# Kernel tuning notes

Measured on AMD Instinct MI355X. Metric: run time of the kernel, lower is better.

Reference implementation:

```python
import jax, jax.numpy as jnp
import numpy as np

N_LAYER = 4
N_HEAD = 12
D_MODEL = 768
SEQ_LEN = 2048
VOCAB = 50257
BATCH = 2


def _sinusoid_pe(seq_len, d_model):
    pos = np.arange(seq_len, dtype=np.float32)[:, None]
    div = np.exp(np.arange(0, d_model, 2, dtype=np.float32) * (-np.log(10000.0) / d_model))
    pe = np.zeros((seq_len, d_model), dtype=np.float32)
    pe[:, 0::2] = np.sin(pos * div)
    pe[:, 1::2] = np.cos(pos * div)
    return jnp.asarray(pe[None])  # [1, C, D]


def setup_inputs() -> dict:
    key = jax.random.key(0)
    ks = jax.random.split(key, 12)
    s = 0.02
    return {
        "features": jax.random.randint(ks[0], (BATCH, SEQ_LEN), 0, VOCAB),
        "targets": jax.random.randint(ks[1], (BATCH, SEQ_LEN), 0, VOCAB),
        "tok_embed": jax.random.normal(ks[2], (VOCAB, D_MODEL), jnp.float32) * s,
        "pos_emb": _sinusoid_pe(SEQ_LEN, D_MODEL),
        "ln1_w": jnp.ones((N_LAYER, D_MODEL), jnp.float32),
        "ln1_b": jnp.zeros((N_LAYER, D_MODEL), jnp.float32),
        "attn_w": jax.random.normal(ks[3], (N_LAYER, D_MODEL, 3 * D_MODEL), jnp.float32) * s,
        "attn_b": jnp.zeros((N_LAYER, 3 * D_MODEL), jnp.float32),
        "proj_w": jax.random.normal(ks[4], (N_LAYER, D_MODEL, D_MODEL), jnp.float32) * s,
        "proj_b": jnp.zeros((N_LAYER, D_MODEL), jnp.float32),
        "ln2_w": jnp.ones((N_LAYER, D_MODEL), jnp.float32),
        "ln2_b": jnp.zeros((N_LAYER, D_MODEL), jnp.float32),
        "ffn_w1": jax.random.normal(ks[5], (N_LAYER, D_MODEL, 4 * D_MODEL), jnp.float32) * s,
        "ffn_b1": jnp.zeros((N_LAYER, 4 * D_MODEL), jnp.float32),
        "ffn_w2": jax.random.normal(ks[6], (N_LAYER, 4 * D_MODEL, D_MODEL), jnp.float32) * s,
        "ffn_b2": jnp.zeros((N_LAYER, D_MODEL), jnp.float32),
        "lnf_w": jnp.ones((D_MODEL,), jnp.float32),
        "lnf_b": jnp.zeros((D_MODEL,), jnp.float32),
        "final_w": jax.random.normal(ks[7], (D_MODEL, VOCAB), jnp.float32) * s,
    }


def _layernorm(x, w, b, eps=1e-5):
    mu = jnp.mean(x, axis=-1, keepdims=True)
    var = jnp.var(x, axis=-1, keepdims=True)
    return (x - mu) * jax.lax.rsqrt(var + eps) * w + b


def _attention(x, wqkv, bqkv, wo, bo):
    B, C, E = x.shape
    dh = E // N_HEAD
    qkv = x @ wqkv + bqkv  # [B, C, 3E]
    q, k, v = jnp.split(qkv, 3, axis=-1)
    q = q.reshape(B, C, N_HEAD, dh)
    k = k.reshape(B, C, N_HEAD, dh)
    v = v.reshape(B, C, N_HEAD, dh)
    att = jnp.einsum("bqhd,bkhd->bhqk", q, k) / jnp.sqrt(jnp.float32(dh))
    causal = jnp.tril(jnp.ones((C, C), bool))
    att = jnp.where(causal, att, -jnp.inf)
    att = jax.nn.softmax(att, axis=-1)
    y = jnp.einsum("bhqk,bkhd->bqhd", att, v).reshape(B, C, E)
    return y @ wo + bo


def reference(features, targets, tok_embed, pos_emb, ln1_w, ln1_b, attn_w, attn_b,
              proj_w, proj_b, ln2_w, ln2_b, ffn_w1, ffn_b1, ffn_w2, ffn_b2,
              lnf_w, lnf_b, final_w):
    C = features.shape[1]
    x = tok_embed[features] + pos_emb[:, :C]
    for l in range(N_LAYER):
        h = _layernorm(x, ln1_w[l], ln1_b[l])
        x = x + _attention(h, attn_w[l], attn_b[l], proj_w[l], proj_b[l])
        h = _layernorm(x, ln2_w[l], ln2_b[l])
        h = jax.nn.gelu(h @ ffn_w1[l] + ffn_b1[l], approximate=False) @ ffn_w2[l] + ffn_b2[l]
        x = x + h
    x = _layernorm(x, lnf_w, lnf_b)
    logits = x @ final_w  # [B, C, V]
    logp = jax.nn.log_softmax(logits, axis=-1)
    tgt = targets.reshape(-1)
    valid = tgt != -1
    tgt_safe = jnp.where(valid, tgt, 0)
    nll = -jnp.take_along_axis(logp.reshape(-1, logits.shape[-1]), tgt_safe[:, None], axis=1)[:, 0]
    loss = jnp.sum(jnp.where(valid, nll, 0.0)) / jnp.maximum(jnp.sum(valid), 1)
    return logits, loss
```

## Files before the change

### kernel.cpp

```cpp
#include <hip/hip_runtime.h>
#include <math.h>

#define N_LAYER 4
#define N_HEAD  12
#define D_MODEL 768
#define SEQ     2048
#define VOCAB   50257
#define BATCH   2
#define MROWS   (BATCH*SEQ)

typedef __bf16 bf16;
typedef __bf16 bf16x8 __attribute__((ext_vector_type(8)));
typedef float  f32x4  __attribute__((ext_vector_type(4)));
typedef short  short8v __attribute__((ext_vector_type(8)));

__device__ __forceinline__ void gload16(const bf16* g, const bf16* l) {
    __builtin_amdgcn_global_load_lds(
        (const __attribute__((address_space(1))) void*)g,
        (__attribute__((address_space(3))) void*)l,
        16, 0, 0);
}

__global__ __launch_bounds__(256) void embed_kernel(
    const int* __restrict__ feat, const float* __restrict__ tok,
    const float* __restrict__ pos, float* __restrict__ x)
{
    int row = blockIdx.x;
    int cpos = row & (SEQ - 1);
    int tid = feat[row];
    const float* te = tok + (size_t)tid * D_MODEL;
    const float* pe = pos + (size_t)cpos * D_MODEL;
    float* xr = x + (size_t)row * D_MODEL;
    for (int c = threadIdx.x; c < D_MODEL; c += 256)
        xr[c] = te[c] + pe[c];
}

__global__ __launch_bounds__(256) void ln_kernel(
    const float* __restrict__ x, const float* __restrict__ w,
    const float* __restrict__ b, bf16* __restrict__ out)
{
    int row = blockIdx.x;
    const float* xr = x + (size_t)row * D_MODEL;
    float lv[3];
    float s = 0.f, ss = 0.f;
#pragma unroll
    for (int i = 0; i < 3; i++) {
        float v = xr[threadIdx.x + i * 256];
        lv[i] = v; s += v; ss += v * v;
    }
#pragma unroll
    for (int o = 32; o; o >>= 1) { s += __shfl_down(s, o, 64); ss += __shfl_down(ss, o, 64); }
    __shared__ float red[8];
    int wid = threadIdx.x >> 6;
    if ((threadIdx.x & 63) == 0) { red[wid] = s; red[wid + 4] = ss; }
    __syncthreads();
    s  = red[0] + red[1] + red[2] + red[3];
    ss = red[4] + red[5] + red[6] + red[7];
    float mu  = s * (1.f / D_MODEL);
    float var = ss * (1.f / D_MODEL) - mu * mu;
    float rs  = rsqrtf(var + 1e-5f);
#pragma unroll
    for (int i = 0; i < 3; i++) {
        int c = threadIdx.x + i * 256;
        out[(size_t)row * D_MODEL + c] = (bf16)((lv[i] - mu) * rs * w[c] + b[c]);
    }
}

__global__ __launch_bounds__(256) void transpose_conv_kernel(
    const float* __restrict__ W, bf16* __restrict__ Wt, int K, int N)
{
    int l = blockIdx.z;
    const float* Wl = W + (size_t)l * K * N;
    bf16* Wtl = Wt + (size_t)l * K * N;
    __shared__ float tile[32][33];
    int k0 = blockIdx.y * 32, n0 = blockIdx.x * 32;
    for (int idx = threadIdx.x; idx < 1024; idx += 256) {
        int i = idx >> 5, j = idx & 31;
        int n = n0 + j;
        tile[i][j] = (n < N) ? Wl[(size_t)(k0 + i) * N + n] : 0.f;
    }
    __syncthreads();
    for (int idx = threadIdx.x; idx < 1024; idx += 256) {
        int j = idx >> 5, i = idx & 31;
        int n = n0 + j;
        if (n < N) Wtl[(size_t)n * K + k0 + i] = (bf16)tile[i][j];
    }
}

__global__ __launch_bounds__(256) void vtrans_kernel(
    const bf16* __restrict__ qkv, bf16* __restrict__ vT)
{
    int j0 = blockIdx.x * 64, h = blockIdx.y, b = blockIdx.z;
    __shared__ bf16 t[64][72];
    const bf16* src = qkv + ((size_t)b * SEQ + j0) * (3 * D_MODEL) + 2 * D_MODEL + h * 64;
    int tid = threadIdx.x;
#pragma unroll
    for (int i = 0; i < 2; i++) {
        int c = tid + i * 256;
        int j = c >> 3, d8 = (c & 7) * 8;
        *(short8v*)&t[j][d8] = *(const short8v*)&src[(size_t)j * (3 * D_MODEL) + d8];
    }
    __syncthreads();
    bf16* dst = vT + ((size_t)(b * N_HEAD + h) * 64) * SEQ;
#pragma unroll
    for (int i = 0; i < 2; i++) {
        int c = tid + i * 256;
        int d = c >> 3, j8 = (c & 7) * 8;
        bf16 tmp[8];
#pragma unroll
        for (int e = 0; e < 8; e++) tmp[e] = t[j8 + e][d];
        *(short8v*)&dst[(size_t)d * SEQ + j0 + j8] = *(const short8v*)tmp;
    }
}

template<bool BIAS, bool GELU_, int OUTM, int SPLITK, bool SWZ, bool LSE>
__global__ __launch_bounds__(256) void gemm_kernel(
    const bf16* __restrict__ A, const bf16* __restrict__ Bt,
    const float* __restrict__ bias, void* __restrict__ Cout,
    float* __restrict__ rowsum,
    int M, int N, int K)
{
    __shared__ __align__(16) bf16 As[2][128 * 32];
    __shared__ __align__(16) bf16 Bs[2][128 * 32];
    int tid = threadIdx.x;
    int lane = tid & 63, wid = tid >> 6;

    int Kslice = K / SPLITK;
    int kbase = (SPLITK > 1) ? (int)blockIdx.z * Kslice : 0;

    int nbx = gridDim.x;
    int bid = blockIdx.y * nbx + blockIdx.x;
    if (SWZ) {
        int nwg = nbx * gridDim.y;
        int q = nwg >> 3, r = nwg & 7;
        int xcd = bid & 7, loc = bid >> 3;
        bid = (xcd < r ? xcd * (q + 1) : r * (q + 1) + (xcd - r) * q) + loc;
    }
    int row0 = (bid % nbx) * 128;
    int col0 = (bid / nbx) * 128;

    int wr = (wid >> 1) * 64, wc = (wid & 1) * 64;

    int srow = wid * 16 + (lane >> 2);
    int selem = (lane & 3) * 8;
    const bf16* Ab0 = A + (size_t)(row0 + srow) * K + kbase + selem;
    const bf16* Ab1 = Ab0 + (size_t)64 * K;
    int bn0 = col0 + srow;      if (bn0 >= N) bn0 = N - 1;
    int bn1 = col0 + srow + 64; if (bn1 >= N) bn1 = N - 1;
    const bf16* Bb0 = Bt + (size_t)bn0 * K + kbase + selem;
    const bf16* Bb1 = Bt + (size_t)bn1 * K + kbase + selem;

    const int nt = Kslice >> 5;
    int fr = lane & 15, fg8 = (lane >> 4) * 8;

    auto stage = [&](int t, int b) {
        int k0 = t * 32;
        gload16(Ab0 + k0, As[b] + wid * 512);
        gload16(Ab1 + k0, As[b] + (wid + 4) * 512);
        gload16(Bb0 + k0, Bs[b] + wid * 512);
        gload16(Bb1 + k0, Bs[b] + (wid + 4) * 512);
    };

    f32x4 acc[4][4] = {};
    stage(0, 0);

    for (int t = 0; t < nt; ++t) {
        int cur = t & 1;
        if (t + 1 < nt) {
            stage(t + 1, cur ^ 1);
            asm volatile("s_waitcnt vmcnt(4)" ::: "memory");
        } else {
            asm volatile("s_waitcnt vmcnt(0)" ::: "memory");
        }
        __builtin_amdgcn_s_barrier();

        bf16x8 af[4], bfr[4];
#pragma unroll
        for (int m = 0; m < 4; m++) af[m] = *(const bf16x8*)&As[cur][(wr + m * 16 + fr) * 32 + fg8];
#pragma unroll
        for (int n = 0; n < 4; n++) bfr[n] = *(const bf16x8*)&Bs[cur][(wc + n * 16 + fr) * 32 + fg8];
#pragma unroll
        for (int m = 0; m < 4; m++)
#pragma unroll
            for (int n = 0; n < 4; n++)
                acc[m][n] = __builtin_amdgcn_mfma_f32_16x16x32_bf16(af[m], bfr[n], acc[m][n], 0, 0, 0);

        asm volatile("s_waitcnt lgkmcnt(0)" ::: "memory");
        __builtin_amdgcn_s_barrier();
    }

    int g = lane >> 4;
    bool addbias = BIAS && (SPLITK == 1 || blockIdx.z == 0);
    float lsum[4][4];
    if (LSE) {
#pragma unroll
        for (int m = 0; m < 4; m++)
#pragma unroll
            for (int r = 0; r < 4; r++) lsum[m][r] = 0.f;
    }

#pragma unroll
    for (int m = 0; m < 4; m++) {
#pragma unroll
        for (int n = 0; n < 4; n++) {
            int col = col0 + wc + n * 16 + fr;
            bool ok = (col < N);
            float bv = (addbias && ok) ? bias[col] : 0.f;
#pragma unroll
            for (int r = 0; r < 4; r++) {
                int row = row0 + wr + m * 16 + g * 4 + r;
                float v = acc[m][n][r] + bv;
                if (GELU_) v = 0.5f * v * (1.f + erff(v * 0.70710678118f));
                if (ok) {
                    if (OUTM == 0)
                        ((float*)Cout)[(size_t)row * N + col] = v;
                    else if (OUTM == 1)
                        ((bf16*)Cout)[(size_t)row * N + col] = (bf16)v;
                    else if (SPLITK > 1)
                        atomicAdd(&((float*)Cout)[(size_t)row * N + col], v);
                    else
                        ((float*)Cout)[(size_t)row * N + col] += v;
                }
                if (LSE) lsum[m][r] += ok ? __expf(v) : 0.f;
            }
        }
    }

    if (LSE) {
#pragma unroll
        for (int m = 0; m < 4; m++)
#pragma unroll
            for (int r = 0; r < 4; r++) {
                float s = lsum[m][r];
#pragma unroll
                for (int o = 1; o < 16; o <<= 1) s += __shfl_xor(s, o, 64);
                lsum[m][r] = s;
            }
        if (fr == 0) {
#pragma unroll
            for (int m = 0; m < 4; m++)
#pragma unroll
                for (int r = 0; r < 4; r++)
                    atomicAdd(&rowsum[row0 + wr + m * 16 + g * 4 + r], lsum[m][r]);
        }
    }
}

__global__ __launch_bounds__(256) void attn_kernel(
    const bf16* __restrict__ qkv, const bf16* __restrict__ vT, bf16* __restrict__ y)
{
    int qt = (int)(gridDim.x - 1 - blockIdx.x), h = blockIdx.y, b = blockIdx.z;
    const size_t rs = 3 * D_MODEL;
    int tid = threadIdx.x, lane = tid & 63, wid = tid >> 6;
    int fr = lane & 15, g = lane >> 4;
    int wq = qt * 64 + wid * 16;

    const bf16* qb = qkv + (size_t)b * SEQ * rs + h * 64;
    const bf16* kb = qb + D_MODEL;
    const bf16* vb = vT + ((size_t)(b * N_HEAD + h) * 64) * SEQ;

    __shared__ bf16 Ps[4][16][72];

    bf16x8 aq[2];
#pragma unroll
    for (int kk = 0; kk < 2; kk++)
        aq[kk] = *(const bf16x8*)&qb[(size_t)(wq + fr) * rs + kk * 32 + g * 8];

    f32x4 acco[4] = {};
    float mrow[4], lrow[4];
#pragma unroll
    for (int r = 0; r < 4; r++) { mrow[r] = -1e30f; lrow[r] = 0.f; }

    int jmax = qt * 64;
    for (int j0 = 0; j0 <= jmax; j0 += 64) {
        f32x4 accs[4] = {};
#pragma unroll
        for (int n = 0; n < 4; n++)
#pragma unroll
            for (int kk = 0; kk < 2; kk++) {
                bf16x8 bk = *(const bf16x8*)&kb[(size_t)(j0 + n * 16 + fr) * rs + kk * 32 + g * 8];
                accs[n] = __builtin_amdgcn_mfma_f32_16x16x32_bf16(aq[kk], bk, accs[n], 0, 0, 0);
            }

        bool diag = (j0 == jmax);
#pragma unroll
        for (int n = 0; n < 4; n++) {
            int jc = j0 + n * 16 + fr;
#pragma unroll
            for (int r = 0; r < 4; r++) {
                float sv = accs[n][r] * 0.125f;
                if (diag) { int irow = wq + g * 4 + r; if (jc > irow) sv = -1e30f; }
                accs[n][r] = sv;
            }
        }

        float pscale[4];
#pragma unroll
        for (int r = 0; r < 4; r++) {
            float pm = fmaxf(fmaxf(accs[0][r], accs[1][r]), fmaxf(accs[2][r], accs[3][r]));
#pragma unroll
            for (int o = 1; o < 16; o <<= 1) pm = fmaxf(pm, __shfl_xor(pm, o, 64));
            float mnew = fmaxf(mrow[r], pm);
            float corr = __expf(mrow[r] - mnew);
            mrow[r] = mnew;
            float ls = 0.f;
#pragma unroll
            for (int n = 0; n < 4; n++) {
                float p = __expf(accs[n][r] - mnew);
                accs[n][r] = p; ls += p;
            }
#pragma unroll
            for (int o = 1; o < 16; o <<= 1) ls += __shfl_xor(ls, o, 64);
            lrow[r] = lrow[r] * corr + ls;
            pscale[r] = corr;
        }
#pragma unroll
        for (int n = 0; n < 4; n++)
#pragma unroll
            for (int r = 0; r < 4; r++) acco[n][r] *= pscale[r];

#pragma unroll
        for (int n = 0; n < 4; n++)
#pragma unroll
            for (int r = 0; r < 4; r++)
                Ps[wid][g * 4 + r][n * 16 + fr] = (bf16)accs[n][r];

        bf16x8 ap[2];
#pragma unroll
        for (int kk = 0; kk < 2; kk++)
            ap[kk] = *(const bf16x8*)&Ps[wid][fr][kk * 32 + g * 8];
#pragma unroll
        for (int kk = 0; kk < 2; kk++)
#pragma unroll
            for (int n = 0; n < 4; n++) {
                bf16x8 bv = *(const bf16x8*)&vb[(size_t)(n * 16 + fr) * SEQ + j0 + kk * 32 + g * 8];
                acco[n] = __builtin_amdgcn_mfma_f32_16x16x32_bf16(ap[kk], bv, acco[n], 0, 0, 0);
            }
    }

    bf16* yb = y + (size_t)b * SEQ * D_MODEL + h * 64;
#pragma unroll
    for (int n = 0; n < 4; n++)
#pragma unroll
        for (int r = 0; r < 4; r++) {
            int row = wq + g * 4 + r;
            yb[(size_t)row * D_MODEL + n * 16 + fr] = (bf16)(acco[n][r] / lrow[r]);
        }
}

__global__ __launch_bounds__(256) void loss_nll_kernel(
    const float* __restrict__ logits, const float* __restrict__ rowsum,
    const int* __restrict__ tgt, float* __restrict__ accum)
{
    int row = blockIdx.x * 256 + threadIdx.x;
    if (row >= MROWS) return;
    int t = tgt[row];
    if (t >= 0) {
        float nll = logf(rowsum[row]) - logits[(size_t)row * VOCAB + t];
        atomicAdd(accum, nll);
        atomicAdd(accum + 1, 1.f);
    }
}

__global__ void loss_final_kernel(const float* __restrict__ accum, float* __restrict__ out)
{
    out[0] = accum[0] / fmaxf(accum[1], 1.f);
}

extern "C" void kernel_launch(void* const* d_in, const int* in_sizes, int n_in,
                              void* d_out, int out_size, void* d_ws, size_t ws_size,
                              hipStream_t stream)
{
    const int*   feat  = (const int*)d_in[0];
    const int*   tgt   = (const int*)d_in[1];
    const float* tok   = (const float*)d_in[2];
    const float* pos   = (const float*)d_in[3];
    const float* ln1w  = (const float*)d_in[4];
    const float* ln1b  = (const float*)d_in[5];
    const float* attnw = (const float*)d_in[6];
    const float* attnb = (const float*)d_in[7];
    const float* projw = (const float*)d_in[8];
    const float* projb = (const float*)d_in[9];
    const float* ln2w  = (const float*)d_in[10];
    const float* ln2b  = (const float*)d_in[11];
    const float* fw1   = (const float*)d_in[12];
    const float* fb1   = (const float*)d_in[13];
    const float* fw2   = (const float*)d_in[14];
    const float* fb2   = (const float*)d_in[15];
    const float* lnfw  = (const float*)d_in[16];
    const float* lnfb  = (const float*)d_in[17];
    const float* finw  = (const float*)d_in[18];

    char* ws = (char*)d_ws;
    size_t off = 0;
    auto alloc = [&](size_t bytes) -> void* {
        void* p = ws + off; off += (bytes + 255) & ~(size_t)255; return p;
    };
    float* x     = (float*)alloc((size_t)MROWS * D_MODEL * 4);
    bf16*  h     = (bf16*) alloc((size_t)MROWS * D_MODEL * 2);
    bf16*  big   = (bf16*) alloc((size_t)MROWS * 4 * D_MODEL * 2);
    bf16*  ybuf  = (bf16*) alloc((size_t)MROWS * D_MODEL * 2);
    bf16*  vT    = (bf16*) alloc((size_t)BATCH * N_HEAD * 64 * SEQ * 2);
    bf16*  awt   = (bf16*) alloc((size_t)N_LAYER * 3 * D_MODEL * D_MODEL * 2);
    bf16*  pwt   = (bf16*) alloc((size_t)N_LAYER * D_MODEL * D_MODEL * 2);
    bf16*  f1wt  = (bf16*) alloc((size_t)N_LAYER * 4 * D_MODEL * D_MODEL * 2);
    bf16*  f2wt  = (bf16*) alloc((size_t)N_LAYER * 4 * D_MODEL * D_MODEL * 2);
    bf16*  fwt   = (bf16*) alloc((size_t)VOCAB * D_MODEL * 2);
    float* rowsum= (float*)alloc((size_t)MROWS * 4);
    float* accum = (float*)alloc(256);

    float* logits = (float*)d_out;
    float* lossp  = (float*)d_out + (size_t)MROWS * VOCAB;

    dim3 blk(256);
    transpose_conv_kernel<<<dim3(3 * D_MODEL / 32, D_MODEL / 32, N_LAYER), blk, 0, stream>>>(attnw, awt, D_MODEL, 3 * D_MODEL);
    transpose_conv_kernel<<<dim3(D_MODEL / 32, D_MODEL / 32, N_LAYER), blk, 0, stream>>>(projw, pwt, D_MODEL, D_MODEL);
    transpose_conv_kernel<<<dim3(4 * D_MODEL / 32, D_MODEL / 32, N_LAYER), blk, 0, stream>>>(fw1, f1wt, D_MODEL, 4 * D_MODEL);
    transpose_conv_kernel<<<dim3(D_MODEL / 32, 4 * D_MODEL / 32, N_LAYER), blk, 0, stream>>>(fw2, f2wt, 4 * D_MODEL, D_MODEL);
    transpose_conv_kernel<<<dim3((VOCAB + 31) / 32, D_MODEL / 32, 1), blk, 0, stream>>>(finw, fwt, D_MODEL, VOCAB);

    embed_kernel<<<MROWS, blk, 0, stream>>>(feat, tok, pos, x);

    for (int l = 0; l < N_LAYER; l++) {
        ln_kernel<<<MROWS, blk, 0, stream>>>(x, ln1w + l * D_MODEL, ln1b + l * D_MODEL, h);
        gemm_kernel<true, false, 1, 1, false, false><<<dim3(MROWS / 128, (3 * D_MODEL) / 128), blk, 0, stream>>>(
            h, awt + (size_t)l * 3 * D_MODEL * D_MODEL, attnb + l * 3 * D_MODEL, big, nullptr,
            MROWS, 3 * D_MODEL, D_MODEL);
        vtrans_kernel<<<dim3(SEQ / 64, N_HEAD, BATCH), blk, 0, stream>>>(big, vT);
        attn_kernel<<<dim3(SEQ / 64, N_HEAD, BATCH), blk, 0, stream>>>(big, vT, ybuf);
        gemm_kernel<true, false, 2, 2, false, false><<<dim3(MROWS / 128, D_MODEL / 128, 2), blk, 0, stream>>>(
            ybuf, pwt + (size_t)l * D_MODEL * D_MODEL, projb + l * D_MODEL, x, nullptr,
            MROWS, D_MODEL, D_MODEL);
        ln_kernel<<<MROWS, blk, 0, stream>>>(x, ln2w + l * D_MODEL, ln2b + l * D_MODEL, h);
        gemm_kernel<true, true, 1, 1, false, false><<<dim3(MROWS / 128, (4 * D_MODEL) / 128), blk, 0, stream>>>(
            h, f1wt + (size_t)l * 4 * D_MODEL * D_MODEL, fb1 + l * 4 * D_MODEL, big, nullptr,
            MROWS, 4 * D_MODEL, D_MODEL);
        gemm_kernel<true, false, 2, 2, false, false><<<dim3(MROWS / 128, D_MODEL / 128, 2), blk, 0, stream>>>(
            big, f2wt + (size_t)l * 4 * D_MODEL * D_MODEL, fb2 + l * D_MODEL, x, nullptr,
            MROWS, D_MODEL, 4 * D_MODEL);
    }

    ln_kernel<<<MROWS, blk, 0, stream>>>(x, lnfw, lnfb, h);

    hipMemsetAsync(rowsum, 0, (size_t)MROWS * 4, stream);
    hipMemsetAsync(accum, 0, 8, stream);

    gemm_kernel<false, false, 0, 1, true, true><<<dim3(MROWS / 128, (VOCAB + 127) / 128), blk, 0, stream>>>(
        h, fwt, nullptr, logits, rowsum, MROWS, VOCAB, D_MODEL);

    loss_nll_kernel<<<(MROWS + 255) / 256, blk, 0, stream>>>(logits, rowsum, tgt, accum);
    loss_final_kernel<<<1, 1, 0, stream>>>(accum, lossp);

    (void)in_sizes; (void)n_in; (void)out_size; (void)ws_size;
}
```

Before: 2.143 ms.

## Add dedicated 256x256-tile 8-wave logits GEMM with fused row exp-sum

Replaces the generic 128x128 GEMM used for the vocab projection with a specialized kernel using 256x256 tiles, 512 threads and BK=64. It double-buffers A and B, issuing async global-to-LDS loads in quarter-steps interleaved with MFMA phases, and raises wave priority around the MFMA blocks. The larger tile is meant to improve data reuse and compute density on the dominant logits GEMM, which is large (4096x50257x768) and writes a lot of output. It drops the XCD swizzle and uses much more LDS (128KB) per block, which risks occupancy and tail-tile waste on the last vocab column.

```diff
diff --git a/kernel.cpp b/kernel.cpp
--- a/kernel.cpp
+++ b/kernel.cpp
@@ -113,11 +113,10 @@
     }
 }
 
-template<bool BIAS, bool GELU_, int OUTM, int SPLITK, bool SWZ, bool LSE>
+template<bool BIAS, bool GELU_, int OUTM, int SPLITK>
 __global__ __launch_bounds__(256) void gemm_kernel(
     const bf16* __restrict__ A, const bf16* __restrict__ Bt,
     const float* __restrict__ bias, void* __restrict__ Cout,
-    float* __restrict__ rowsum,
     int M, int N, int K)
 {
     __shared__ __align__(16) bf16 As[2][128 * 32];
@@ -128,16 +127,8 @@
     int Kslice = K / SPLITK;
     int kbase = (SPLITK > 1) ? (int)blockIdx.z * Kslice : 0;
 
-    int nbx = gridDim.x;
-    int bid = blockIdx.y * nbx + blockIdx.x;
-    if (SWZ) {
-        int nwg = nbx * gridDim.y;
-        int q = nwg >> 3, r = nwg & 7;
-        int xcd = bid & 7, loc = bid >> 3;
-        bid = (xcd < r ? xcd * (q + 1) : r * (q + 1) + (xcd - r) * q) + loc;
-    }
-    int row0 = (bid % nbx) * 128;
-    int col0 = (bid / nbx) * 128;
+    int row0 = blockIdx.x * 128;
+    int col0 = blockIdx.y * 128;
 
     int wr = (wid >> 1) * 64, wc = (wid & 1) * 64;
 
@@ -191,13 +182,6 @@
 
     int g = lane >> 4;
     bool addbias = BIAS && (SPLITK == 1 || blockIdx.z == 0);
-    float lsum[4][4];
-    if (LSE) {
-#pragma unroll
-        for (int m = 0; m < 4; m++)
-#pragma unroll
-            for (int r = 0; r < 4; r++) lsum[m][r] = 0.f;
-    }
 
 #pragma unroll
     for (int m = 0; m < 4; m++) {
@@ -221,27 +205,176 @@
                     else
                         ((float*)Cout)[(size_t)row * N + col] += v;
                 }
-                if (LSE) lsum[m][r] += ok ? __expf(v) : 0.f;
             }
         }
     }
-
-    if (LSE) {
-#pragma unroll
-        for (int m = 0; m < 4; m++)
+}
+
+__global__ __launch_bounds__(512, 2) void gemm256_logits_kernel(
+    const bf16* __restrict__ A, const bf16* __restrict__ Bt,
+    float* __restrict__ Cout, float* __restrict__ rowsum, int N, int K)
+{
+    __shared__ __align__(16) bf16 As[2][256 * 64];
+    __shared__ __align__(16) bf16 Bs[2][256 * 64];
+    int tid = threadIdx.x, lane = tid & 63, wid = tid >> 6;
+    int wm = wid >> 2, wn = wid & 3;
+    int row0 = blockIdx.x * 256, col0 = blockIdx.y * 256;
+    int fr = lane & 15, fg8 = (lane >> 4) * 8, g = lane >> 4;
+
+    int srow_c = lane >> 3;
+    int scol   = (lane & 7) * 8;
+
+    const int nt = K >> 6;
+
+    auto stageA = [&](int t, int half) {
+        int buf = t & 1, k0 = t * 64;
+#pragma unroll
+        for (int j = 0; j < 2; j++) {
+            int rloc = half * 128 + (wid * 2 + j) * 8;
+            gload16(A + (size_t)(row0 + rloc + srow_c) * K + k0 + scol,
+                    As[buf] + rloc * 64);
+        }
+    };
+    auto stageB = [&](int t, int half) {
+        int buf = t & 1, k0 = t * 64;
+#pragma unroll
+        for (int j = 0; j < 2; j++) {
+            int rloc = half * 128 + (wid * 2 + j) * 8;
+            int grow = col0 + rloc + srow_c;
+            if (grow >= N) grow = N - 1;
+            gload16(Bt + (size_t)grow * K + k0 + scol,
+                    Bs[buf] + rloc * 64);
+        }
+    };
+
+    f32x4 acc[8][4] = {};
+
+    stageA(0, 0); stageA(0, 1); stageB(0, 0); stageB(0, 1);
+    stageB(1, 0); stageB(1, 1);
+    asm volatile("s_waitcnt vmcnt(4)" ::: "memory");
+    __builtin_amdgcn_s_barrier();
+
+    for (int t = 0; t < nt; ++t) {
+        int c = t & 1;
+        const bf16* Ac = As[c];
+        const bf16* Bc = Bs[c];
+
+        bf16x8 bfrag[4][2];
+#pragma unroll
+        for (int n = 0; n < 4; n++)
+#pragma unroll
+            for (int ks = 0; ks < 2; ks++)
+                bfrag[n][ks] = *(const bf16x8*)&Bc[(wn * 64 + n * 16 + fr) * 64 + ks * 32 + fg8];
+        {
+            bf16x8 a_[2][2];
+#pragma unroll
+            for (int mi = 0; mi < 2; mi++)
+#pragma unroll
+                for (int ks = 0; ks < 2; ks++)
+                    a_[mi][ks] = *(const bf16x8*)&Ac[(wm * 128 + mi * 16 + fr) * 64 + ks * 32 + fg8];
+            if (t + 1 < nt) stageA(t + 1, 0);
+            __builtin_amdgcn_s_barrier();
+            __builtin_amdgcn_s_setprio(1);
+#pragma unroll
+            for (int mi = 0; mi < 2; mi++)
+#pragma unroll
+                for (int n = 0; n < 4; n++)
+#pragma unroll
+                    for (int ks = 0; ks < 2; ks++)
+                        acc[mi][n] = __builtin_amdgcn_mfma_f32_16x16x32_bf16(a_[mi][ks], bfrag[n][ks], acc[mi][n], 0, 0, 0);
+            __builtin_amdgcn_s_setprio(0);
+            __builtin_amdgcn_s_barrier();
+        }
+        {
+            bf16x8 a_[2][2];
+#pragma unroll
+            for (int mi = 0; mi < 2; mi++)
+#pragma unroll
+                for (int ks = 0; ks < 2; ks++)
+                    a_[mi][ks] = *(const bf16x8*)&Ac[(wm * 128 + (2 + mi) * 16 + fr) * 64 + ks * 32 + fg8];
+            if (t + 1 < nt) stageA(t + 1, 1);
+            if (t + 2 < nt) stageB(t + 2, 0);
+            __builtin_amdgcn_s_barrier();
+            __builtin_amdgcn_s_setprio(1);
+#pragma unroll
+            for (int mi = 0; mi < 2; mi++)
+#pragma unroll
+                for (int n = 0; n < 4; n++)
+#pragma unroll
+                    for (int ks = 0; ks < 2; ks++)
+                        acc[2 + mi][n] = __builtin_amdgcn_mfma_f32_16x16x32_bf16(a_[mi][ks], bfrag[n][ks], acc[2 + mi][n], 0, 0, 0);
+            __builtin_amdgcn_s_setprio(0);
+            __builtin_amdgcn_s_barrier();
+        }
+        {
+            bf16x8 a_[2][2];
+#pragma unroll
+            for (int mi = 0; mi < 2; mi++)
+#pragma unroll
+                for (int ks = 0; ks < 2; ks++)
+                    a_[mi][ks] = *(const bf16x8*)&Ac[(wm * 128 + (4 + mi) * 16 + fr) * 64 + ks * 32 + fg8];
+            if (t + 2 < nt) stageB(t + 2, 1);
+            __builtin_amdgcn_s_barrier();
+            __builtin_amdgcn_s_setprio(1);
+#pragma unroll
+            for (int mi = 0; mi < 2; mi++)
+#pragma unroll
+                for (int n = 0; n < 4; n++)
+#pragma unroll
+                    for (int ks = 0; ks < 2; ks++)
+                        acc[4 + mi][n] = __builtin_amdgcn_mfma_f32_16x16x32_bf16(a_[mi][ks], bfrag[n][ks], acc[4 + mi][n], 0, 0, 0);
+            __builtin_amdgcn_s_setprio(0);
+            __builtin_amdgcn_s_barrier();
+        }
+        {
+            bf16x8 a_[2][2];
+#pragma unroll
+            for (int mi = 0; mi < 2; mi++)
+#pragma unroll
+                for (int ks = 0; ks < 2; ks++)
+                    a_[mi][ks] = *(const bf16x8*)&Ac[(wm * 128 + (6 + mi) * 16 + fr) * 64 + ks * 32 + fg8];
+            __builtin_amdgcn_s_barrier();
+            __builtin_amdgcn_s_setprio(1);
+#pragma unroll
+            for (int mi = 0; mi < 2; mi++)
+#pragma unroll
+                for (int n = 0; n < 4; n++)
+#pragma unroll
+                    for (int ks = 0; ks < 2; ks++)
+                        acc[6 + mi][n] = __builtin_amdgcn_mfma_f32_16x16x32_bf16(a_[mi][ks], bfrag[n][ks], acc[6 + mi][n], 0, 0, 0);
+            __builtin_amdgcn_s_setprio(0);
+            if (t + 2 < nt)
+                asm volatile("s_waitcnt vmcnt(4)" ::: "memory");
+            else if (t + 1 < nt)
+                asm volatile("s_waitcnt vmcnt(0)" ::: "memory");
+            __builtin_amdgcn_s_barrier();
+        }
+    }
+
+#pragma unroll
+    for (int mf = 0; mf < 8; mf++) {
+        float lsum[4] = {0.f, 0.f, 0.f, 0.f};
+#pragma unroll
+        for (int n = 0; n < 4; n++) {
+            int col = col0 + wn * 64 + n * 16 + fr;
+            bool ok = (col < N);
 #pragma unroll
             for (int r = 0; r < 4; r++) {
-                float s = lsum[m][r];
-#pragma unroll
-                for (int o = 1; o < 16; o <<= 1) s += __shfl_xor(s, o, 64);
-                lsum[m][r] = s;
+                int row = row0 + wm * 128 + mf * 16 + g * 4 + r;
+                float v = acc[mf][n][r];
+                if (ok) {
+                    Cout[(size_t)row * N + col] = v;
+                    lsum[r] += __expf(v);
+                }
             }
-        if (fr == 0) {
-#pragma unroll
-            for (int m = 0; m < 4; m++)
-#pragma unroll
-                for (int r = 0; r < 4; r++)
-                    atomicAdd(&rowsum[row0 + wr + m * 16 + g * 4 + r], lsum[m][r]);
+        }
+#pragma unroll
+        for (int r = 0; r < 4; r++) {
+            float s = lsum[r];
+#pragma unroll
+            for (int o = 1; o < 16; o <<= 1) s += __shfl_xor(s, o, 64);
+            if (fr == 0)
+                atomicAdd(&rowsum[row0 + wm * 128 + mf * 16 + g * 4 + r], s);
         }
     }
 }
@@ -423,20 +556,20 @@
 
     for (int l = 0; l < N_LAYER; l++) {
         ln_kernel<<<MROWS, blk, 0, stream>>>(x, ln1w + l * D_MODEL, ln1b + l * D_MODEL, h);
-        gemm_kernel<true, false, 1, 1, false, false><<<dim3(MROWS / 128, (3 * D_MODEL) / 128), blk, 0, stream>>>(
-            h, awt + (size_t)l * 3 * D_MODEL * D_MODEL, attnb + l * 3 * D_MODEL, big, nullptr,
+        gemm_kernel<true, false, 1, 1><<<dim3(MROWS / 128, (3 * D_MODEL) / 128), blk, 0, stream>>>(
+            h, awt + (size_t)l * 3 * D_MODEL * D_MODEL, attnb + l * 3 * D_MODEL, big,
             MROWS, 3 * D_MODEL, D_MODEL);
         vtrans_kernel<<<dim3(SEQ / 64, N_HEAD, BATCH), blk, 0, stream>>>(big, vT);
         attn_kernel<<<dim3(SEQ / 64, N_HEAD, BATCH), blk, 0, stream>>>(big, vT, ybuf);
-        gemm_kernel<true, false, 2, 2, false, false><<<dim3(MROWS / 128, D_MODEL / 128, 2), blk, 0, stream>>>(
-            ybuf, pwt + (size_t)l * D_MODEL * D_MODEL, projb + l * D_MODEL, x, nullptr,
+        gemm_kernel<true, false, 2, 2><<<dim3(MROWS / 128, D_MODEL / 128, 2), blk, 0, stream>>>(
+            ybuf, pwt + (size_t)l * D_MODEL * D_MODEL, projb + l * D_MODEL, x,
             MROWS, D_MODEL, D_MODEL);
         ln_kernel<<<MROWS, blk, 0, stream>>>(x, ln2w + l * D_MODEL, ln2b + l * D_MODEL, h);
-        gemm_kernel<true, true, 1, 1, false, false><<<dim3(MROWS / 128, (4 * D_MODEL) / 128), blk, 0, stream>>>(
-            h, f1wt + (size_t)l * 4 * D_MODEL * D_MODEL, fb1 + l * 4 * D_MODEL, big, nullptr,
+        gemm_kernel<true, true, 1, 1><<<dim3(MROWS / 128, (4 * D_MODEL) / 128), blk, 0, stream>>>(
+            h, f1wt + (size_t)l * 4 * D_MODEL * D_MODEL, fb1 + l * 4 * D_MODEL, big,
             MROWS, 4 * D_MODEL, D_MODEL);
-        gemm_kernel<true, false, 2, 2, false, false><<<dim3(MROWS / 128, D_MODEL / 128, 2), blk, 0, stream>>>(
-            big, f2wt + (size_t)l * 4 * D_MODEL * D_MODEL, fb2 + l * D_MODEL, x, nullptr,
+        gemm_kernel<true, false, 2, 2><<<dim3(MROWS / 128, D_MODEL / 128, 2), blk, 0, stream>>>(
+            big, f2wt + (size_t)l * 4 * D_MODEL * D_MODEL, fb2 + l * D_MODEL, x,
             MROWS, D_MODEL, 4 * D_MODEL);
     }
 
@@ -445,8 +578,8 @@
     hipMemsetAsync(rowsum, 0, (size_t)MROWS * 4, stream);
     hipMemsetAsync(accum, 0, 8, stream);
 
-    gemm_kernel<false, false, 0, 1, true, true><<<dim3(MROWS / 128, (VOCAB + 127) / 128), blk, 0, stream>>>(
-        h, fwt, nullptr, logits, rowsum, MROWS, VOCAB, D_MODEL);
+    gemm256_logits_kernel<<<dim3(MROWS / 256, (VOCAB + 255) / 256), dim3(512), 0, stream>>>(
+        h, fwt, logits, rowsum, VOCAB, D_MODEL);
 
     loss_nll_kernel<<<(MROWS + 255) / 256, blk, 0, stream>>>(logits, rowsum, tgt, accum);
     loss_final_kernel<<<1, 1, 0, stream>>>(accum, lossp);
```

New measurement: 2.159 ms. About the same (+0.7%).
